# Kernel optimization log

Measured on AMD Instinct MI355X. Metric: run time of the kernel, lower is better.

## Reference

```python
import jax, jax.numpy as jnp
import numpy as np

N, C, F = 2048, 512, 512

def setup_inputs() -> dict:
    key = jax.random.key(0)
    k1, k2 = jax.random.split(key)
    x = jax.random.normal(k1, (N, F), dtype=jnp.float32)
    means = jax.random.normal(k2, (C, F), dtype=jnp.float32)
    return {"x": x, "means": means}

def reference(x, means):
    # Negative squared Euclidean distance from each sample to each class mean.
    # diff: (N, C, F) broadcasted; output: (N, C)
    diff = x[:, None, :] - means[None, :, :]
    return -jnp.sum(diff * diff, axis=-1)
```

## Files before the change

### kernel.cpp

```cpp
#include <hip/hip_runtime.h>
#include <hip/hip_bf16.h>


#define F_DIM  512
#define C_ROWS 512

typedef __attribute__((ext_vector_type(8))) short short8;
typedef __attribute__((ext_vector_type(4))) float f32x4;

static __device__ __forceinline__ short f2bf_rne(float f) {
    unsigned u = __builtin_bit_cast(unsigned, f);
    unsigned r = (u + 0x7fffu + ((u >> 16) & 1u)) >> 16;
    return (short)r;
}

__global__ __launch_bounds__(256) void ncm_fused(
        const float* __restrict__ x, const float* __restrict__ means,
        float* __restrict__ out) {
    __shared__ __align__(16) short As[64 * 512];
    __shared__ __align__(16) short Bs[64 * 512];
    __shared__ float xn_s[64], mn_s[64];

    const int d  = blockIdx.x;
    const int by = (d & 7) * 4 + ((d >> 3) & 3);
    const int bx = d >> 5;
    const int rowBase = by * 64, colBase = bx * 64;

    const int t    = threadIdx.x;
    const int w    = t >> 6;
    const int lane = t & 63;
    const int qr   = lane >> 4;
    const int ql   = lane & 15;

#pragma unroll
    for (int half = 0; half < 2; half++) {
        const float* src = (half == 0) ? x + (size_t)rowBase * F_DIM
                                       : means + (size_t)colBase * F_DIM;
        short* dst = (half == 0) ? As : Bs;
        float* nrm = (half == 0) ? xn_s : mn_s;

        float4 va[4][4][2];
#pragma unroll
        for (int i = 0; i < 4; i++) {
            const int r = w * 16 + i * 4 + qr;
            const float* rowp = src + (size_t)r * F_DIM;
#pragma unroll
            for (int ph = 0; ph < 4; ph++) {
                const float* p = rowp + ph * 128 + ql * 8;
                va[i][ph][0] = *(const float4*)p;
                va[i][ph][1] = *(const float4*)(p + 4);
            }
        }
#pragma unroll
        for (int i = 0; i < 4; i++) {
            const int r = w * 16 + i * 4 + qr;
            float ss = 0.f;
#pragma unroll
            for (int ph = 0; ph < 4; ph++) {
                float vv[8] = {va[i][ph][0].x, va[i][ph][0].y,
                               va[i][ph][0].z, va[i][ph][0].w,
                               va[i][ph][1].x, va[i][ph][1].y,
                               va[i][ph][1].z, va[i][ph][1].w};
                short8 o;
#pragma unroll
                for (int j = 0; j < 8; j++) {
                    ss += vv[j] * vv[j];
                    o[j] = f2bf_rne(vv[j]);
                }
                const int slot = ph * 16 + ql;
                *(short8*)(dst + r * F_DIM + ((slot ^ (r & 7)) << 3)) = o;
            }
            ss += __shfl_xor(ss, 1);
            ss += __shfl_xor(ss, 2);
            ss += __shfl_xor(ss, 4);
            ss += __shfl_xor(ss, 8);
            if (ql == 0) nrm[r] = ss;
        }
    }
    __syncthreads();

    const int wr = (w >> 1) * 32;
    const int wc = (w & 1) * 32;

    f32x4 acc[2][2];
#pragma unroll
    for (int mi = 0; mi < 2; mi++)
#pragma unroll
        for (int ni = 0; ni < 2; ni++)
            acc[mi][ni] = (f32x4){0.f, 0.f, 0.f, 0.f};

#pragma unroll
    for (int kk = 0; kk < 16; kk++) {
        const int slot = kk * 4 + (lane >> 4);
        short8 a[2], b[2];
#pragma unroll
        for (int mi = 0; mi < 2; mi++) {
            const int r = wr + mi * 16 + (lane & 15);
            a[mi] = *(const short8*)(As + r * F_DIM + ((slot ^ (r & 7)) << 3));
        }
#pragma unroll
        for (int ni = 0; ni < 2; ni++) {
            const int r = wc + ni * 16 + (lane & 15);
            b[ni] = *(const short8*)(Bs + r * F_DIM + ((slot ^ (r & 7)) << 3));
        }
#pragma unroll
        for (int mi = 0; mi < 2; mi++)
#pragma unroll
            for (int ni = 0; ni < 2; ni++)
                acc[mi][ni] = __builtin_amdgcn_mfma_f32_16x16x32_bf16(
                    a[mi], b[ni], acc[mi][ni], 0, 0, 0);
    }

    float xn[2][4];
#pragma unroll
    for (int mi = 0; mi < 2; mi++)
#pragma unroll
        for (int j = 0; j < 4; j++)
            xn[mi][j] = xn_s[wr + mi * 16 + (lane >> 4) * 4 + j];

#pragma unroll
    for (int ni = 0; ni < 2; ni++) {
        const int cl = wc + ni * 16 + (lane & 15);
        const int c  = colBase + cl;
        const float mn = mn_s[cl];
#pragma unroll
        for (int mi = 0; mi < 2; mi++) {
            const int rbase = rowBase + wr + mi * 16 + (lane >> 4) * 4;
#pragma unroll
            for (int j = 0; j < 4; j++)
                out[(size_t)(rbase + j) * C_ROWS + c] =
                    2.0f * acc[mi][ni][j] - xn[mi][j] - mn;
        }
    }
}

extern "C" void kernel_launch(void* const* d_in, const int* in_sizes, int n_in,
                              void* d_out, int out_size, void* d_ws, size_t ws_size,
                              hipStream_t stream) {
    const float* x     = (const float*)d_in[0];
    const float* means = (const float*)d_in[1];
    float* out = (float*)d_out;
    ncm_fused<<<256, 256, 0, stream>>>(x, means, out);
}
```

Baseline: 12.99 us.

## Double block threads and split K across wave pairs with LDS reduction

Raises the block to 512 threads (8 waves). Each wave now loads and converts half as many rows during staging. In the MFMA phase, two groups of four waves each cover half of the K dimension, and the partial accumulators are combined through shared memory (reusing the A tile buffer) before the epilogue. The aim is more latency hiding in the load/convert phase and a shorter serial MFMA chain per wave. The cost is two extra barriers and an LDS round-trip for the reduction, and half the waves sit idle during the epilogue.

Measured after the change: 11.48 us. 11.6% less time.

```diff
diff --git a/kernel.cpp b/kernel.cpp
--- a/kernel.cpp
+++ b/kernel.cpp
@@ -14,7 +14,7 @@
     return (short)r;
 }
 
-__global__ __launch_bounds__(256) void ncm_fused(
+__global__ __launch_bounds__(512) void ncm_fused(
         const float* __restrict__ x, const float* __restrict__ means,
         float* __restrict__ out) {
     __shared__ __align__(16) short As[64 * 512];
@@ -39,10 +39,10 @@
         short* dst = (half == 0) ? As : Bs;
         float* nrm = (half == 0) ? xn_s : mn_s;
 
-        float4 va[4][4][2];
+        float4 va[2][4][2];
 #pragma unroll
-        for (int i = 0; i < 4; i++) {
-            const int r = w * 16 + i * 4 + qr;
+        for (int i = 0; i < 2; i++) {
+            const int r = w * 8 + i * 4 + qr;
             const float* rowp = src + (size_t)r * F_DIM;
 #pragma unroll
             for (int ph = 0; ph < 4; ph++) {
@@ -52,8 +52,8 @@
             }
         }
 #pragma unroll
-        for (int i = 0; i < 4; i++) {
-            const int r = w * 16 + i * 4 + qr;
+        for (int i = 0; i < 2; i++) {
+            const int r = w * 8 + i * 4 + qr;
             float ss = 0.f;
 #pragma unroll
             for (int ph = 0; ph < 4; ph++) {
@@ -79,8 +79,10 @@
     }
     __syncthreads();
 
-    const int wr = (w >> 1) * 32;
-    const int wc = (w & 1) * 32;
+    const int quad = w & 3;
+    const int kh   = w >> 2;
+    const int wr   = (quad >> 1) * 32;
+    const int wc   = (quad & 1) * 32;
 
     f32x4 acc[2][2];
 #pragma unroll
@@ -90,7 +92,8 @@
             acc[mi][ni] = (f32x4){0.f, 0.f, 0.f, 0.f};
 
 #pragma unroll
-    for (int kk = 0; kk < 16; kk++) {
+    for (int j = 0; j < 8; j++) {
+        const int kk   = kh * 8 + j;
         const int slot = kk * 4 + (lane >> 4);
         short8 a[2], b[2];
 #pragma unroll
@@ -111,25 +114,49 @@
                     a[mi], b[ni], acc[mi][ni], 0, 0, 0);
     }
 
-    float xn[2][4];
+    __syncthreads();
+    float* red = (float*)As;
+    if (kh == 1) {
 #pragma unroll
-    for (int mi = 0; mi < 2; mi++)
+        for (int mi = 0; mi < 2; mi++)
 #pragma unroll
-        for (int j = 0; j < 4; j++)
-            xn[mi][j] = xn_s[wr + mi * 16 + (lane >> 4) * 4 + j];
+            for (int ni = 0; ni < 2; ni++)
+#pragma unroll
+                for (int j = 0; j < 4; j++)
+                    red[quad * 1088 + lane * 17 + mi * 8 + ni * 4 + j] =
+                        acc[mi][ni][j];
+    }
+    __syncthreads();
+    if (kh == 0) {
+#pragma unroll
+        for (int mi = 0; mi < 2; mi++)
+#pragma unroll
+            for (int ni = 0; ni < 2; ni++)
+#pragma unroll
+                for (int j = 0; j < 4; j++)
+                    acc[mi][ni][j] +=
+                        red[quad * 1088 + lane * 17 + mi * 8 + ni * 4 + j];
+
+        float xn[2][4];
+#pragma unroll
+        for (int mi = 0; mi < 2; mi++)
+#pragma unroll
+            for (int j = 0; j < 4; j++)
+                xn[mi][j] = xn_s[wr + mi * 16 + (lane >> 4) * 4 + j];
 
 #pragma unroll
-    for (int ni = 0; ni < 2; ni++) {
-        const int cl = wc + ni * 16 + (lane & 15);
-        const int c  = colBase + cl;
-        const float mn = mn_s[cl];
+        for (int ni = 0; ni < 2; ni++) {
+            const int cl = wc + ni * 16 + (lane & 15);
+            const int c  = colBase + cl;
+            const float mn = mn_s[cl];
 #pragma unroll
-        for (int mi = 0; mi < 2; mi++) {
-            const int rbase = rowBase + wr + mi * 16 + (lane >> 4) * 4;
+            for (int mi = 0; mi < 2; mi++) {
+                const int rbase = rowBase + wr + mi * 16 + (lane >> 4) * 4;
 #pragma unroll
-            for (int j = 0; j < 4; j++)
-                out[(size_t)(rbase + j) * C_ROWS + c] =
-                    2.0f * acc[mi][ni][j] - xn[mi][j] - mn;
+                for (int j = 0; j < 4; j++)
+                    out[(size_t)(rbase + j) * C_ROWS + c] =
+                        2.0f * acc[mi][ni][j] - xn[mi][j] - mn;
+            }
         }
     }
 }
@@ -140,5 +167,5 @@
     const float* x     = (const float*)d_in[0];
     const float* means = (const float*)d_in[1];
     float* out = (float*)d_out;
-    ncm_fused<<<256, 256, 0, stream>>>(x, means, out);
+    ncm_fused<<<256, 512, 0, stream>>>(x, means, out);
 }
```
